# Kernel optimization log

Hardware: AMD Instinct MI355X
Metric: run time of the kernel (lower is better)

Reference implementation:

```python
import jax, jax.numpy as jnp
import numpy as np

# Module hyperparameters (from init_kwargs)
START = 0.0      # lower distance cutoff
STOP = 5.0       # radius_graph cutoff r
K = 32           # max_num_neighbors
N_ATOMS = 16384
N_GRAPHS = 64
BOX = 30.0       # box edge length (Angstrom) -> realistic density for r=5 cutoff


def setup_inputs() -> dict:
    key = jax.random.key(0)
    k1, k2 = jax.random.split(key)
    pos = jax.random.uniform(k1, (N_ATOMS, 3), dtype=jnp.float32) * BOX
    batch = jnp.sort(jax.random.randint(k2, (N_ATOMS,), 0, N_GRAPHS)).astype(jnp.int64)
    return {"pos": pos, "batch": batch}


def reference(pos, batch):
    """radius_graph (loop=False) + edge vectors/norms + lower-cutoff mask.

    Because jit requires static shapes, the variable-length edge list of the
    original is returned in padded form: edge_index [2, N*K], edge_weight [N*K],
    edge_vec [N*K, 3], plus a boolean validity mask [N*K]. Valid entries match
    the original (edge_index, edge_weight, edge_vec) after compaction.
    """
    N = pos.shape[0]
    # Pairwise squared distances via the Gram trick: [N, N], memory-bound.
    sq = jnp.sum(pos * pos, axis=-1)
    d2 = sq[:, None] + sq[None, :] - 2.0 * (pos @ pos.T)
    idx = jnp.arange(N)
    valid = (batch[:, None] == batch[None, :]) \
            & (idx[:, None] != idx[None, :]) \
            & (d2 <= STOP * STOP)
    d2m = jnp.where(valid, d2, jnp.inf)
    # Up to K nearest neighbors within the radius per node.
    neg_d2, nbr = jax.lax.top_k(-d2m, K)          # [N, K]
    nbr_valid = neg_d2 > -jnp.inf                  # in-radius, same-graph, non-self
    nbr = jnp.where(nbr_valid, nbr, idx[:, None])  # pad with self (vec = 0)
    # edge_vec = pos[center] - pos[neighbor]  (pos[edge_index[0]] - pos[edge_index[1]])
    edge_vec = pos[:, None, :] - pos[nbr]          # [N, K, 3]
    sqd = jnp.sum(edge_vec * edge_vec, axis=-1)
    w = jnp.where(nbr_valid, jnp.sqrt(jnp.where(nbr_valid, sqd, 1.0)), 0.0)
    lower = nbr_valid & (w >= START)               # lower cutoff mask
    src = jnp.broadcast_to(idx[:, None], (N, K))
    edge_index = jnp.stack([src.reshape(-1), nbr.reshape(-1)])  # [2, N*K]
    mask = lower.reshape(-1)
    edge_weight = jnp.where(lower, w, 0.0).reshape(-1)
    edge_vec = jnp.where(lower[..., None], edge_vec, 0.0).reshape(-1, 3)
    return edge_index, edge_weight, edge_vec, mask
```

## Files before the change

### kernel.cpp

```cpp
#include <hip/hip_runtime.h>
#include <math.h>

#define KNBR 32
#define STOP2 25.0
#define CAP 128
#define WPB 4

__global__ __launch_bounds__(WPB * 64)
void radius_graph_knn(const float* __restrict__ pos,
                      const int* __restrict__ batch,
                      float* __restrict__ out, int n) {
    __shared__ double d2buf[WPB][CAP];
    __shared__ int    jbuf[WPB][CAP];
    __shared__ int    win[WPB][KNBR];

    const int lane = threadIdx.x & 63;
    const int w    = threadIdx.x >> 6;
    const int i    = blockIdx.x * WPB + w;
    const int ic   = (i < n) ? i : (n - 1);

    const float xi = pos[3 * ic];
    const float yi = pos[3 * ic + 1];
    const float zi = pos[3 * ic + 2];
    const double xid = (double)xi, yid = (double)yi, zid = (double)zi;
    const int b = batch[ic];

    const int nchunks = (n + 63) >> 6;
    const int c0 = ic >> 6;
    const int cw = c0 - 32 + lane;
    bool rel = false;
    if (cw >= 0 && cw < nchunks) {
        const int s = batch[cw << 6];
        const int e = batch[min(n - 1, (cw << 6) + 63)];
        rel = (s <= b) && (e >= b);
    }
    const unsigned long long cm = __ballot(rel);
    const int cLo = c0 - 32 + __builtin_ctzll(cm);
    const int cHi = c0 - 32 + (63 - __builtin_clzll(cm));

    int count = 0;
    for (int c = cLo; c <= cHi; ++c) {
        const int j  = (c << 6) + lane;
        const int jj = min(j, n - 1);
        const int bj = batch[jj];
        const double dx = xid - (double)pos[3 * jj];
        const double dy = yid - (double)pos[3 * jj + 1];
        const double dz = zid - (double)pos[3 * jj + 2];
        const double d2 = dx * dx + dy * dy + dz * dz;
        const bool valid = (j < n) & (j != ic) & (bj == b) & (d2 <= STOP2);
        const unsigned long long m = __ballot(valid);
        const int p = count + __popcll(m & ((1ULL << lane) - 1ULL));
        if (valid && p < CAP) { d2buf[w][p] = d2; jbuf[w][p] = j; }
        count += __popcll(m);
    }
    if (count > CAP) count = CAP;
    const int nsel = count < KNBR ? count : KNBR;

    __syncthreads();

    for (int t = lane; t < count; t += 64) {
        const double dt = d2buf[w][t];
        const int    jt = jbuf[w][t];
        int rank = 0;
        for (int s = 0; s < count; ++s) {
            const double ds = d2buf[w][s];
            const int    js = jbuf[w][s];
            rank += (ds < dt || (ds == dt && js < jt)) ? 1 : 0;
        }
        if (rank < KNBR) win[w][rank] = jt;
    }

    __syncthreads();

    const long long NK = (long long)n * KNBR;
    float* row0 = out;
    float* row1 = out + NK;
    float* wgt  = out + 2 * NK;
    float* vec  = out + 3 * NK;
    float* msk  = out + 6 * NK;
    const long long obase = (long long)ic * KNBR;

    if (i < n && lane < KNBR) {
        const int s = lane;
        const bool v = (s < nsel);
        const int j = v ? win[w][s] : ic;
        const float vx = xi - pos[3 * j];
        const float vy = yi - pos[3 * j + 1];
        const float vz = zi - pos[3 * j + 2];
        const float ww = v ? sqrtf(vx * vx + vy * vy + vz * vz) : 0.0f;
        row0[obase + s] = (float)ic;
        row1[obase + s] = (float)j;
        wgt[obase + s]  = ww;
        vec[3 * (obase + s) + 0] = v ? vx : 0.0f;
        vec[3 * (obase + s) + 1] = v ? vy : 0.0f;
        vec[3 * (obase + s) + 2] = v ? vz : 0.0f;
        msk[obase + s]  = v ? 1.0f : 0.0f;
    }
}

extern "C" void kernel_launch(void* const* d_in, const int* in_sizes, int n_in,
                              void* d_out, int out_size, void* d_ws, size_t ws_size,
                              hipStream_t stream) {
    const float* pos   = (const float*)d_in[0];
    const int*   batch = (const int*)d_in[1];
    float* out = (float*)d_out;
    int n = in_sizes[1];

    const int block = WPB * 64;
    const int grid = (n + WPB - 1) / WPB;
    radius_graph_knn<<<grid, block, 0, stream>>>(pos, batch, out, n);
}
```

Before: 71.81 us.

## Stage candidate atoms in shared memory and rank neighbors via wave shuffles

The block now loads the union of relevant candidate chunks for its four atoms into LDS once, as float4 holding position and batch id, and shares them across waves instead of each wave reading global memory. Candidates are filtered in fp32 with a small tolerance band, and only the survivors are rechecked in fp64. Ranking moves from a shared-memory O(count²) loop to register shuffles within the wave, which removes two block barriers. The change adds a CAND_CAP=768 staging limit and reduces the per-atom candidate cap to 64, which can truncate results for large graphs or dense neighborhoods.

```diff
diff --git a/kernel.cpp b/kernel.cpp
--- a/kernel.cpp
+++ b/kernel.cpp
@@ -3,74 +3,100 @@
 
 #define KNBR 32
 #define STOP2 25.0
-#define CAP 128
+#define BAND 1.0e-3f
+#define CAND_CAP 768
+#define CAP 64
 #define WPB 4
 
 __global__ __launch_bounds__(WPB * 64)
 void radius_graph_knn(const float* __restrict__ pos,
                       const int* __restrict__ batch,
                       float* __restrict__ out, int n) {
-    __shared__ double d2buf[WPB][CAP];
+    __shared__ float4 cand[CAND_CAP];
     __shared__ int    jbuf[WPB][CAP];
     __shared__ int    win[WPB][KNBR];
 
-    const int lane = threadIdx.x & 63;
-    const int w    = threadIdx.x >> 6;
-    const int i    = blockIdx.x * WPB + w;
-    const int ic   = (i < n) ? i : (n - 1);
+    const int tid  = threadIdx.x;
+    const int lane = tid & 63;
+    const int w    = tid >> 6;
+    const int i0   = blockIdx.x * WPB;
+    const int i    = min(i0 + w, n - 1);
 
-    const float xi = pos[3 * ic];
-    const float yi = pos[3 * ic + 1];
-    const float zi = pos[3 * ic + 2];
-    const double xid = (double)xi, yid = (double)yi, zid = (double)zi;
-    const int b = batch[ic];
-
+    const int bFirst = batch[i0];
+    const int bLast  = batch[min(i0 + WPB - 1, n - 1)];
     const int nchunks = (n + 63) >> 6;
-    const int c0 = ic >> 6;
+    const int c0 = i0 >> 6;
     const int cw = c0 - 32 + lane;
     bool rel = false;
     if (cw >= 0 && cw < nchunks) {
         const int s = batch[cw << 6];
         const int e = batch[min(n - 1, (cw << 6) + 63)];
-        rel = (s <= b) && (e >= b);
+        rel = (s <= bLast) && (e >= bFirst);
     }
     const unsigned long long cm = __ballot(rel);
-    const int cLo = c0 - 32 + __builtin_ctzll(cm);
-    const int cHi = c0 - 32 + (63 - __builtin_clzll(cm));
+    const int cLo = c0 - 32 + (int)__builtin_ctzll(cm);
+    const int cHi = c0 - 32 + (63 - (int)__builtin_clzll(cm));
+    const int base = cLo << 6;
+    int stagedN = min(n, (cHi + 1) << 6) - base;
+    if (stagedN > CAND_CAP) stagedN = CAND_CAP;
+
+    for (int t = tid; t < stagedN; t += WPB * 64) {
+        const int j = base + t;
+        float4 c;
+        c.x = pos[3 * j];
+        c.y = pos[3 * j + 1];
+        c.z = pos[3 * j + 2];
+        c.w = __int_as_float(batch[j]);
+        cand[t] = c;
+    }
+    __syncthreads();
+
+    const float4 self = cand[i - base];
+    const float xi = self.x, yi = self.y, zi = self.z;
+    const int b = __float_as_int(self.w);
+    const double xid = xi, yid = yi, zid = zi;
 
     int count = 0;
-    for (int c = cLo; c <= cHi; ++c) {
-        const int j  = (c << 6) + lane;
-        const int jj = min(j, n - 1);
-        const int bj = batch[jj];
-        const double dx = xid - (double)pos[3 * jj];
-        const double dy = yid - (double)pos[3 * jj + 1];
-        const double dz = zid - (double)pos[3 * jj + 2];
-        const double d2 = dx * dx + dy * dy + dz * dz;
-        const bool valid = (j < n) & (j != ic) & (bj == b) & (d2 <= STOP2);
+    for (int t0 = 0; t0 < stagedN; t0 += 64) {
+        const int t = t0 + lane;
+        const int tc = min(t, stagedN - 1);
+        const float4 c = cand[tc];
+        const float dx = xi - c.x, dy = yi - c.y, dz = zi - c.z;
+        const float d2 = dx * dx + dy * dy + dz * dz;
+        const int j = base + tc;
+        const bool valid = (t < stagedN) & (j != i) &
+                           (__float_as_int(c.w) == b) & (d2 <= 25.0f + BAND);
         const unsigned long long m = __ballot(valid);
         const int p = count + __popcll(m & ((1ULL << lane) - 1ULL));
-        if (valid && p < CAP) { d2buf[w][p] = d2; jbuf[w][p] = j; }
+        if (valid && p < CAP) jbuf[w][p] = tc;
         count += __popcll(m);
     }
     if (count > CAP) count = CAP;
-    const int nsel = count < KNBR ? count : KNBR;
 
-    __syncthreads();
-
-    for (int t = lane; t < count; t += 64) {
-        const double dt = d2buf[w][t];
-        const int    jt = jbuf[w][t];
-        int rank = 0;
-        for (int s = 0; s < count; ++s) {
-            const double ds = d2buf[w][s];
-            const int    js = jbuf[w][s];
-            rank += (ds < dt || (ds == dt && js < jt)) ? 1 : 0;
-        }
-        if (rank < KNBR) win[w][rank] = jt;
+    double d2e = 1e300;
+    int jmine = 0x7fffffff, slot = 0;
+    bool valid = false;
+    if (lane < count) {
+        slot = jbuf[w][lane];
+        const float4 c = cand[slot];
+        const double dx = xid - (double)c.x;
+        const double dy = yid - (double)c.y;
+        const double dz = zid - (double)c.z;
+        d2e = dx * dx + dy * dy + dz * dz;
+        jmine = base + slot;
+        valid = (d2e <= STOP2);
     }
-
-    __syncthreads();
+    const unsigned long long vm = __ballot(valid);
+    int nsel = __popcll(vm);
+    if (nsel > KNBR) nsel = KNBR;
+    int rank = 0;
+    for (int s = 0; s < count; ++s) {
+        const double ds = __shfl(d2e, s);
+        const int    js = __shfl(jmine, s);
+        const bool   vs = (vm >> s) & 1ULL;
+        rank += (vs && (ds < d2e || (ds == d2e && js < jmine))) ? 1 : 0;
+    }
+    if (valid && rank < KNBR) win[w][rank] = slot;
 
     const long long NK = (long long)n * KNBR;
     float* row0 = out;
@@ -78,17 +104,17 @@
     float* wgt  = out + 2 * NK;
     float* vec  = out + 3 * NK;
     float* msk  = out + 6 * NK;
-    const long long obase = (long long)ic * KNBR;
+    const long long obase = (long long)i * KNBR;
 
-    if (i < n && lane < KNBR) {
+    if ((i0 + w) < n && lane < KNBR) {
         const int s = lane;
         const bool v = (s < nsel);
-        const int j = v ? win[w][s] : ic;
-        const float vx = xi - pos[3 * j];
-        const float vy = yi - pos[3 * j + 1];
-        const float vz = zi - pos[3 * j + 2];
+        const int sl = v ? win[w][s] : (i - base);
+        const float4 c = cand[sl];
+        const int j = base + sl;
+        const float vx = xi - c.x, vy = yi - c.y, vz = zi - c.z;
         const float ww = v ? sqrtf(vx * vx + vy * vy + vz * vz) : 0.0f;
-        row0[obase + s] = (float)ic;
+        row0[obase + s] = (float)i;
         row1[obase + s] = (float)j;
         wgt[obase + s]  = ww;
         vec[3 * (obase + s) + 0] = v ? vx : 0.0f;
```

Measured after the change: 69.02 us. 3.9% less time.
